# Performance work log

Measured on AMD Instinct MI355X. Metric: run time of the kernel, lower is better.

Reference implementation:

```python
import jax, jax.numpy as jnp
import numpy as np

OUT_F = 4096   # compressed rows; logical m = 2*OUT_F
IN_F = 2048    # compressed cols; logical k = 2*IN_F
BATCH = 4096   # n = input.shape[0]

# valid sorted 2-of-4 column patterns for 2:4 structured sparsity
_PAIR_LUT = jnp.array([[0, 1], [0, 2], [0, 3], [1, 2], [1, 3], [2, 3]], dtype=jnp.int32)


def setup_inputs() -> dict:
    key = jax.random.key(0)
    k1, k2, k3, k4 = jax.random.split(key, 4)
    weight = jax.random.normal(k1, (OUT_F, IN_F), dtype=jnp.float32)
    # vector (row) sparsity: keep 1 of every 2 logical row-vectors -> collision-free logical row ids
    row_bit = jax.random.randint(k2, (OUT_F,), 0, 2)
    indices = (2 * jnp.arange(OUT_F, dtype=jnp.int32) + row_bit.astype(jnp.int32))
    # 2:4 column sparsity: per group of 4 logical cols, keep 2 distinct sorted positions
    pat = jax.random.randint(k3, (OUT_F, IN_F // 2), 0, 6)
    metadata = _PAIR_LUT[pat].reshape(OUT_F, IN_F)  # [OUT_F, IN_F], values in 0..3
    inp = jax.random.normal(k4, (BATCH, 2 * IN_F), dtype=jnp.float32)
    return {"weight": weight, "indices": indices, "metadata": metadata, "input": inp}


def reference(weight, indices, metadata, input):
    # Decompress the dual structured-sparse weight to its logical dense form,
    # then compute W_logical @ input^T (spmm_dense_trans semantics).
    out_f, in_f = weight.shape
    m, k = 2 * out_f, 2 * in_f
    # logical column of each compressed element: group base 4*(c//2) + 2-bit metadata
    col = 4 * (jnp.arange(in_f, dtype=jnp.int32) // 2)[None, :] + metadata  # [out_f, in_f]
    W = jnp.zeros((m, k), dtype=weight.dtype).at[indices[:, None], col].set(weight)
    return W @ input.T  # [m, n] = [2*out_f, batch]
```

## Files before the change

### kernel.cpp

```cpp
#include <hip/hip_runtime.h>

#define OUT_F 4096
#define IN_F  2048
#define KLOG  4096
#define NB    4096
typedef unsigned long long ull;
typedef ull ullx2 __attribute__((ext_vector_type(2)));

typedef __bf16 bf16x8 __attribute__((ext_vector_type(8)));
typedef short  s16x8  __attribute__((ext_vector_type(8)));
typedef float  f32x4  __attribute__((ext_vector_type(4)));

__device__ __forceinline__ unsigned short f2bf(float f) {
    unsigned int u = __float_as_uint(f);
    u += 0x7fffu + ((u >> 16) & 1u);
    return (unsigned short)(u >> 16);
}

__device__ __forceinline__ void gload_lds16(const void* g, void* l) {
    __builtin_amdgcn_global_load_lds(
        (const __attribute__((address_space(1))) unsigned int*)g,
        (__attribute__((address_space(3))) unsigned int*)l, 16, 0, 0);
}

__device__ __forceinline__ bf16x8 ldsf(const char* p) {
    return __builtin_bit_cast(bf16x8, *(const s16x8*)p);
}

#define MFMA16(a, b, c) __builtin_amdgcn_mfma_f32_16x16x32_bf16((a), (b), (c), 0, 0, 0)

__global__ __launch_bounds__(256) void prep_kernel(
    const float* __restrict__ weight, const int* __restrict__ metadata,
    const float* __restrict__ input,
    unsigned short* __restrict__ wsA, unsigned short* __restrict__ wsB)
{
    const int b = blockIdx.x;
    if (b < 4096) {
        const int g = b * 256 + threadIdx.x;
        const int r = g >> 8;
        const int c = (g & 255) * 8;
        const size_t off = (size_t)r * IN_F + c;
        const float4 w0 = *(const float4*)(weight + off);
        const float4 w1 = *(const float4*)(weight + off + 4);
        const int4   m0 = *(const int4*)(metadata + off);
        const int4   m1 = *(const int4*)(metadata + off + 4);
        ullx2 v01, v23;
        v01.x = ((ull)f2bf(w0.x) << (m0.x * 16)) | ((ull)f2bf(w0.y) << (m0.y * 16));
        v01.y = ((ull)f2bf(w0.z) << (m0.z * 16)) | ((ull)f2bf(w0.w) << (m0.w * 16));
        v23.x = ((ull)f2bf(w1.x) << (m1.x * 16)) | ((ull)f2bf(w1.y) << (m1.y * 16));
        v23.y = ((ull)f2bf(w1.z) << (m1.z * 16)) | ((ull)f2bf(w1.w) << (m1.w * 16));
        ull* dst = (ull*)(wsA + (size_t)r * KLOG + 2 * c);
        *(ullx2*)(dst)     = v01;
        *(ullx2*)(dst + 2) = v23;
    } else {
        const int g = (b - 4096) * 256 + threadIdx.x;
        const size_t off = (size_t)g * 16;
        const float4 f0 = *(const float4*)(input + off);
        const float4 f1 = *(const float4*)(input + off + 4);
        const float4 f2 = *(const float4*)(input + off + 8);
        const float4 f3 = *(const float4*)(input + off + 12);
        ullx2 v01, v23;
        v01.x =  (ull)f2bf(f0.x) | ((ull)f2bf(f0.y) << 16) | ((ull)f2bf(f0.z) << 32) | ((ull)f2bf(f0.w) << 48);
        v01.y =  (ull)f2bf(f1.x) | ((ull)f2bf(f1.y) << 16) | ((ull)f2bf(f1.z) << 32) | ((ull)f2bf(f1.w) << 48);
        v23.x =  (ull)f2bf(f2.x) | ((ull)f2bf(f2.y) << 16) | ((ull)f2bf(f2.z) << 32) | ((ull)f2bf(f2.w) << 48);
        v23.y =  (ull)f2bf(f3.x) | ((ull)f2bf(f3.y) << 16) | ((ull)f2bf(f3.z) << 32) | ((ull)f2bf(f3.w) << 48);
        ull* dst = (ull*)(wsB + off);
        *(ullx2*)(dst)     = v01;
        *(ullx2*)(dst + 2) = v23;
    }
}

__global__ __launch_bounds__(512, 2) void gemm_kernel256(
    const unsigned short* __restrict__ wsA, const unsigned short* __restrict__ wsB,
    const int* __restrict__ indices, float* __restrict__ out)
{
    __shared__ __align__(16) char lds[4 * 32768];

    const int tid  = threadIdx.x;
    const int lane = tid & 63;
    const int wave = tid >> 6;
    const int wm   = wave >> 2;
    const int wn   = wave & 3;
    const int l15  = lane & 15;
    const int quad = lane >> 4;

    const int swz = ((blockIdx.x & 7) << 5) | (blockIdx.x >> 3);
    const int r0 = (swz >> 4) << 8;
    const int b0 = (swz & 15) << 8;

    const int srow   = tid >> 2;
    const int schunk = (tid & 3) ^ ((tid >> 3) & 3);
    const unsigned short* gA = wsA + (size_t)(r0 + srow) * KLOG + schunk * 8;
    const unsigned short* gB = wsB + (size_t)(b0 + srow) * KLOG + schunk * 8;
    char* const ldsW = lds + wave * 1024;

    const unsigned xq    = (unsigned)((quad ^ ((l15 >> 1) & 3)) * 16);
    const unsigned aBase = (unsigned)((wm * 128 + l15) * 64);
    const unsigned bBase = (unsigned)((wn * 64  + l15) * 64);

    f32x4 acc[8][4];
#pragma unroll
    for (int i = 0; i < 8; ++i)
#pragma unroll
        for (int j = 0; j < 4; ++j) acc[i][j] = (f32x4){0.f, 0.f, 0.f, 0.f};

#define STAGE_A(t_) do { \
        char* _d = ldsW + (((t_) & 3) * 32768); \
        const unsigned short* _s = gA + (t_) * 32; \
        gload_lds16(_s, _d); \
        gload_lds16(_s + (size_t)128 * KLOG, _d + 8192); } while (0)
#define STAGE_B(t_) do { \
        char* _d = ldsW + (((t_) & 3) * 32768) + 16384; \
        const unsigned short* _s = gB + (t_) * 32; \
        gload_lds16(_s, _d); \
        gload_lds16(_s + (size_t)128 * KLOG, _d + 8192); } while (0)

#define BAR()     __builtin_amdgcn_s_barrier()
#define SCHED0()  __builtin_amdgcn_sched_barrier(0)
#define LGKM0()   asm volatile("s_waitcnt lgkmcnt(0)" ::: "memory")

    STAGE_A(0); STAGE_B(0);
    STAGE_A(1); STAGE_B(1);
    STAGE_A(2); STAGE_B(2);
    asm volatile("s_waitcnt vmcnt(8)" ::: "memory");
    BAR();
    SCHED0();

    for (int t = 0; t < 128; ++t) {
        const unsigned bufO = (unsigned)(t & 3) * 32768u;
        const char* pA = lds + bufO + aBase;
        const char* pB = lds + bufO + 16384u + bBase;

        bf16x8 b0f = ldsf(pB + xq);
        bf16x8 b1f = ldsf(pB + 1024 + xq);
        bf16x8 b2f = ldsf(pB + 2048 + xq);
        bf16x8 b3f = ldsf(pB + 3072 + xq);
        bf16x8 a0 = ldsf(pA + xq);
        bf16x8 a1 = ldsf(pA + 1024 + xq);
        bf16x8 a2 = ldsf(pA + 2048 + xq);
        bf16x8 a3 = ldsf(pA + 3072 + xq);
        if (t < 125) STAGE_A(t + 3);
        BAR();
        LGKM0();
        SCHED0();
        __builtin_amdgcn_s_setprio(1);
        acc[0][0] = MFMA16(a0, b0f, acc[0][0]);
        acc[0][1] = MFMA16(a0, b1f, acc[0][1]);
        acc[0][2] = MFMA16(a0, b2f, acc[0][2]);
        acc[0][3] = MFMA16(a0, b3f, acc[0][3]);
        acc[1][0] = MFMA16(a1, b0f, acc[1][0]);
        acc[1][1] = MFMA16(a1, b1f, acc[1][1]);
        acc[1][2] = MFMA16(a1, b2f, acc[1][2]);
        acc[1][3] = MFMA16(a1, b3f, acc[1][3]);
        acc[2][0] = MFMA16(a2, b0f, acc[2][0]);
        acc[2][1] = MFMA16(a2, b1f, acc[2][1]);
        acc[2][2] = MFMA16(a2, b2f, acc[2][2]);
        acc[2][3] = MFMA16(a2, b3f, acc[2][3]);
        acc[3][0] = MFMA16(a3, b0f, acc[3][0]);
        acc[3][1] = MFMA16(a3, b1f, acc[3][1]);
        acc[3][2] = MFMA16(a3, b2f, acc[3][2]);
        acc[3][3] = MFMA16(a3, b3f, acc[3][3]);
        __builtin_amdgcn_s_setprio(0);
        BAR();
        SCHED0();

        bf16x8 a4 = ldsf(pA + 4096 + xq);
        bf16x8 a5 = ldsf(pA + 5120 + xq);
        bf16x8 a6 = ldsf(pA + 6144 + xq);
        bf16x8 a7 = ldsf(pA + 7168 + xq);
        if (t < 125) STAGE_B(t + 3);
        BAR();
        LGKM0();
        SCHED0();
        __builtin_amdgcn_s_setprio(1);
        acc[4][0] = MFMA16(a4, b0f, acc[4][0]);
        acc[4][1] = MFMA16(a4, b1f, acc[4][1]);
        acc[4][2] = MFMA16(a4, b2f, acc[4][2]);
        acc[4][3] = MFMA16(a4, b3f, acc[4][3]);
        acc[5][0] = MFMA16(a5, b0f, acc[5][0]);
        acc[5][1] = MFMA16(a5, b1f, acc[5][1]);
        acc[5][2] = MFMA16(a5, b2f, acc[5][2]);
        acc[5][3] = MFMA16(a5, b3f, acc[5][3]);
        acc[6][0] = MFMA16(a6, b0f, acc[6][0]);
        acc[6][1] = MFMA16(a6, b1f, acc[6][1]);
        acc[6][2] = MFMA16(a6, b2f, acc[6][2]);
        acc[6][3] = MFMA16(a6, b3f, acc[6][3]);
        acc[7][0] = MFMA16(a7, b0f, acc[7][0]);
        acc[7][1] = MFMA16(a7, b1f, acc[7][1]);
        acc[7][2] = MFMA16(a7, b2f, acc[7][2]);
        acc[7][3] = MFMA16(a7, b3f, acc[7][3]);
        __builtin_amdgcn_s_setprio(0);

        if (t < 125) {
            asm volatile("s_waitcnt vmcnt(8)" ::: "memory");
        } else if (t == 125) {
            asm volatile("s_waitcnt vmcnt(4)" ::: "memory");
        } else if (t == 126) {
            asm volatile("s_waitcnt vmcnt(0)" ::: "memory");
        }
        BAR();
        SCHED0();
    }
#undef STAGE_A
#undef STAGE_B
#undef BAR
#undef SCHED0
#undef LGKM0

#pragma unroll
    for (int rg = 0; rg < 8; ++rg) {
#pragma unroll
        for (int e = 0; e < 4; ++e) {
            const int rloc = wm * 128 + rg * 16 + quad * 4 + e;
            const int L = indices[r0 + rloc];
            const size_t base  = (size_t)L * NB;
            const size_t baseZ = (size_t)(L ^ 1) * NB;
#pragma unroll
            for (int cf = 0; cf < 4; ++cf) {
                const int col = b0 + wn * 64 + cf * 16 + l15;
                out[base  + col] = acc[rg][cf][e];
                out[baseZ + col] = 0.0f;
            }
        }
    }
}

__global__ __launch_bounds__(256) void spmm_dt_fallback(
    const float* __restrict__ weight, const int* __restrict__ indices,
    const int* __restrict__ metadata, const float* __restrict__ input,
    float* __restrict__ out)
{
    __shared__ __align__(16) unsigned short As[128][32];
    __shared__ __align__(16) unsigned short Bs[128][32];
    const int tid = threadIdx.x, lane = tid & 63, wave = tid >> 6;
    const int wm = wave >> 1, wn = wave & 1, l15 = lane & 15, quad = lane >> 4;
    const int r0 = blockIdx.y * 128, b0 = blockIdx.x * 128;
    f32x4 acc[4][4];
#pragma unroll
    for (int i = 0; i < 4; ++i)
#pragma unroll
        for (int j = 0; j < 4; ++j) acc[i][j] = (f32x4){0.f, 0.f, 0.f, 0.f};
    const int srow = tid >> 3, sgrp = tid & 7;
    for (int kk = 0; kk < KLOG / 32; ++kk) {
        const int c0 = kk * 16, k0 = kk * 32;
#pragma unroll
        for (int s = 0; s < 4; ++s) {
            const int row = srow + s * 32;
            const size_t off = (size_t)(r0 + row) * IN_F + c0 + 2 * sgrp;
            const float2 w = *(const float2*)(weight + off);
            const int2  md = *(const int2*)(metadata + off);
            *(ull*)(&As[row][4 * sgrp]) =
                ((ull)f2bf(w.x) << (md.x * 16)) | ((ull)f2bf(w.y) << (md.y * 16));
        }
#pragma unroll
        for (int s = 0; s < 4; ++s) {
            const int row = srow + s * 32;
            const float4 f = *(const float4*)(&input[(size_t)(b0 + row) * KLOG + k0 + sgrp * 4]);
            *(ull*)(&Bs[row][sgrp * 4]) =
                 (ull)f2bf(f.x) | ((ull)f2bf(f.y) << 16) |
                ((ull)f2bf(f.z) << 32) | ((ull)f2bf(f.w) << 48);
        }
        __syncthreads();
        bf16x8 a[4], b[4];
#pragma unroll
        for (int i = 0; i < 4; ++i)
            a[i] = __builtin_bit_cast(bf16x8, *(const s16x8*)(&As[wm * 64 + i * 16 + l15][quad * 8]));
#pragma unroll
        for (int j = 0; j < 4; ++j)
            b[j] = __builtin_bit_cast(bf16x8, *(const s16x8*)(&Bs[wn * 64 + j * 16 + l15][quad * 8]));
#pragma unroll
        for (int i = 0; i < 4; ++i)
#pragma unroll
            for (int j = 0; j < 4; ++j)
                acc[i][j] = __builtin_amdgcn_mfma_f32_16x16x32_bf16(a[i], b[j], acc[i][j], 0, 0, 0);
        __syncthreads();
    }
#pragma unroll
    for (int i = 0; i < 4; ++i)
#pragma unroll
        for (int t = 0; t < 4; ++t) {
            const int r = r0 + wm * 64 + i * 16 + quad * 4 + t;
            const int L = indices[r];
            const size_t base = (size_t)L * NB, baseZ = (size_t)(L ^ 1) * NB;
#pragma unroll
            for (int j = 0; j < 4; ++j) {
                const int col = b0 + wn * 64 + j * 16 + l15;
                out[base + col] = acc[i][j][t];
                out[baseZ + col] = 0.0f;
            }
        }
}

extern "C" void kernel_launch(void* const* d_in, const int* in_sizes, int n_in,
                              void* d_out, int out_size, void* d_ws, size_t ws_size,
                              hipStream_t stream) {
    const float* weight   = (const float*)d_in[0];
    const int*   indices  = (const int*)d_in[1];
    const int*   metadata = (const int*)d_in[2];
    const float* input    = (const float*)d_in[3];
    float*       out      = (float*)d_out;

    const size_t needA = (size_t)OUT_F * KLOG * 2;
    const size_t needB = (size_t)NB * KLOG * 2;
    if (ws_size >= needA + needB) {
        unsigned short* wsA = (unsigned short*)d_ws;
        unsigned short* wsB = wsA + (size_t)OUT_F * KLOG;
        prep_kernel<<<dim3(8192), dim3(256), 0, stream>>>(weight, metadata, input, wsA, wsB);
        gemm_kernel256<<<dim3(256), dim3(512), 0, stream>>>(wsA, wsB, indices, out);
    } else {
        spmm_dt_fallback<<<dim3(NB / 128, OUT_F / 128), dim3(256), 0, stream>>>(
            weight, indices, metadata, input, out);
    }
}
```

Baseline: 354.3 us.

## Pre-swizzle weight into MFMA fragment layout and load A directly to registers

The prep kernel now writes the decompressed bf16 weight in a fragment-ordered layout, so each lane's MFMA A operand is a contiguous 16-byte chunk. The GEMM then loads A straight from global memory into double-buffered registers instead of staging it through LDS, leaving only B in a halved LDS ring. The main loop becomes one barrier-synchronised phase per K tile instead of two. The intent is to cut LDS traffic, barriers and LDS footprint, at the cost of more registers and global-load latency that has to be hidden by the one-tile register prefetch.

```diff
diff --git a/kernel.cpp b/kernel.cpp
--- a/kernel.cpp
+++ b/kernel.cpp
@@ -27,6 +27,10 @@
     return __builtin_bit_cast(bf16x8, *(const s16x8*)p);
 }
 
+__device__ __forceinline__ bf16x8 gldf(const unsigned short* p) {
+    return __builtin_bit_cast(bf16x8, *(const s16x8*)p);
+}
+
 #define MFMA16(a, b, c) __builtin_amdgcn_mfma_f32_16x16x32_bf16((a), (b), (c), 0, 0, 0)
 
 __global__ __launch_bounds__(256) void prep_kernel(
@@ -35,25 +39,22 @@
     unsigned short* __restrict__ wsA, unsigned short* __restrict__ wsB)
 {
     const int b = blockIdx.x;
-    if (b < 4096) {
-        const int g = b * 256 + threadIdx.x;
-        const int r = g >> 8;
-        const int c = (g & 255) * 8;
-        const size_t off = (size_t)r * IN_F + c;
-        const float4 w0 = *(const float4*)(weight + off);
-        const float4 w1 = *(const float4*)(weight + off + 4);
-        const int4   m0 = *(const int4*)(metadata + off);
-        const int4   m1 = *(const int4*)(metadata + off + 4);
-        ullx2 v01, v23;
-        v01.x = ((ull)f2bf(w0.x) << (m0.x * 16)) | ((ull)f2bf(w0.y) << (m0.y * 16));
-        v01.y = ((ull)f2bf(w0.z) << (m0.z * 16)) | ((ull)f2bf(w0.w) << (m0.w * 16));
-        v23.x = ((ull)f2bf(w1.x) << (m1.x * 16)) | ((ull)f2bf(w1.y) << (m1.y * 16));
-        v23.y = ((ull)f2bf(w1.z) << (m1.z * 16)) | ((ull)f2bf(w1.w) << (m1.w * 16));
-        ull* dst = (ull*)(wsA + (size_t)r * KLOG + 2 * c);
-        *(ullx2*)(dst)     = v01;
-        *(ullx2*)(dst + 2) = v23;
+    if (b < 8192) {
+        const int R    = b >> 5;
+        const int lane = threadIdx.x & 63;
+        const int Kq   = ((b & 31) << 2) + (threadIdx.x >> 6);
+        const int row  = (R << 4) + (lane & 15);
+        const int kl0  = (Kq << 5) + (lane >> 4) * 8;
+        const int cc   = kl0 >> 1;
+        const size_t off = (size_t)row * IN_F + cc;
+        const float4 w = *(const float4*)(weight + off);
+        const int4  md = *(const int4*)(metadata + off);
+        ullx2 v;
+        v.x = ((ull)f2bf(w.x) << (md.x * 16)) | ((ull)f2bf(w.y) << (md.y * 16));
+        v.y = ((ull)f2bf(w.z) << (md.z * 16)) | ((ull)f2bf(w.w) << (md.w * 16));
+        *(ullx2*)(wsA + ((size_t)(R * 128 + Kq) * 64 + lane) * 8) = v;
     } else {
-        const int g = (b - 4096) * 256 + threadIdx.x;
+        const int g = (b - 8192) * 256 + threadIdx.x;
         const size_t off = (size_t)g * 16;
         const float4 f0 = *(const float4*)(input + off);
         const float4 f1 = *(const float4*)(input + off + 4);
@@ -71,10 +72,11 @@
 }
 
 __global__ __launch_bounds__(512, 2) void gemm_kernel256(
-    const unsigned short* __restrict__ wsA, const unsigned short* __restrict__ wsB,
+    const unsigned short* __restrict__ wsA,
+    const unsigned short* __restrict__ wsB,
     const int* __restrict__ indices, float* __restrict__ out)
 {
-    __shared__ __align__(16) char lds[4 * 32768];
+    __shared__ __align__(16) char lds[4 * 16384];
 
     const int tid  = threadIdx.x;
     const int lane = tid & 63;
@@ -90,13 +92,13 @@
 
     const int srow   = tid >> 2;
     const int schunk = (tid & 3) ^ ((tid >> 3) & 3);
-    const unsigned short* gA = wsA + (size_t)(r0 + srow) * KLOG + schunk * 8;
     const unsigned short* gB = wsB + (size_t)(b0 + srow) * KLOG + schunk * 8;
-    char* const ldsW = lds + wave * 1024;
 
     const unsigned xq    = (unsigned)((quad ^ ((l15 >> 1) & 3)) * 16);
-    const unsigned aBase = (unsigned)((wm * 128 + l15) * 64);
-    const unsigned bBase = (unsigned)((wn * 64  + l15) * 64);
+    const unsigned bBase = (unsigned)((wn * 64 + l15) * 64);
+
+    const unsigned short* aBase = wsA
+        + (size_t)((r0 >> 4) + wm * 8) * 128 * 512 + (unsigned)lane * 8;
 
     f32x4 acc[8][4];
 #pragma unroll
@@ -104,108 +106,92 @@
 #pragma unroll
         for (int j = 0; j < 4; ++j) acc[i][j] = (f32x4){0.f, 0.f, 0.f, 0.f};
 
-#define STAGE_A(t_) do { \
-        char* _d = ldsW + (((t_) & 3) * 32768); \
-        const unsigned short* _s = gA + (t_) * 32; \
-        gload_lds16(_s, _d); \
-        gload_lds16(_s + (size_t)128 * KLOG, _d + 8192); } while (0)
+    bf16x8 aP[8], aQ[8];
+
 #define STAGE_B(t_) do { \
-        char* _d = ldsW + (((t_) & 3) * 32768) + 16384; \
+        char* _d = lds + (((t_) & 3) * 16384) + wave * 1024; \
         const unsigned short* _s = gB + (t_) * 32; \
         gload_lds16(_s, _d); \
         gload_lds16(_s + (size_t)128 * KLOG, _d + 8192); } while (0)
 
+#define LOADA(D, t_) do { \
+        const unsigned short* _p = aBase + (size_t)(t_) * 512; \
+        D[0] = gldf(_p); \
+        D[1] = gldf(_p + 1 * 65536); \
+        D[2] = gldf(_p + 2 * 65536); \
+        D[3] = gldf(_p + 3 * 65536); \
+        D[4] = gldf(_p + 4 * 65536); \
+        D[5] = gldf(_p + 5 * 65536); \
+        D[6] = gldf(_p + 6 * 65536); \
+        D[7] = gldf(_p + 7 * 65536); } while (0)
+
 #define BAR()     __builtin_amdgcn_s_barrier()
 #define SCHED0()  __builtin_amdgcn_sched_barrier(0)
-#define LGKM0()   asm volatile("s_waitcnt lgkmcnt(0)" ::: "memory")
-
-    STAGE_A(0); STAGE_B(0);
-    STAGE_A(1); STAGE_B(1);
-    STAGE_A(2); STAGE_B(2);
-    asm volatile("s_waitcnt vmcnt(8)" ::: "memory");
+
+#define TILE(t_, CUR, NXT) do { \
+        if ((t_) < 127) LOADA(NXT, (t_) + 1); \
+        if ((t_) < 125) STAGE_B((t_) + 3); \
+        const char* pB = lds + ((unsigned)((t_) & 3)) * 16384u + bBase; \
+        bf16x8 bf0 = ldsf(pB + xq); \
+        bf16x8 bf1 = ldsf(pB + 1024 + xq); \
+        bf16x8 bf2 = ldsf(pB + 2048 + xq); \
+        bf16x8 bf3 = ldsf(pB + 3072 + xq); \
+        SCHED0(); \
+        __builtin_amdgcn_s_setprio(1); \
+        acc[0][0] = MFMA16(CUR[0], bf0, acc[0][0]); \
+        acc[0][1] = MFMA16(CUR[0], bf1, acc[0][1]); \
+        acc[0][2] = MFMA16(CUR[0], bf2, acc[0][2]); \
+        acc[0][3] = MFMA16(CUR[0], bf3, acc[0][3]); \
+        acc[1][0] = MFMA16(CUR[1], bf0, acc[1][0]); \
+        acc[1][1] = MFMA16(CUR[1], bf1, acc[1][1]); \
+        acc[1][2] = MFMA16(CUR[1], bf2, acc[1][2]); \
+        acc[1][3] = MFMA16(CUR[1], bf3, acc[1][3]); \
+        acc[2][0] = MFMA16(CUR[2], bf0, acc[2][0]); \
+        acc[2][1] = MFMA16(CUR[2], bf1, acc[2][1]); \
+        acc[2][2] = MFMA16(CUR[2], bf2, acc[2][2]); \
+        acc[2][3] = MFMA16(CUR[2], bf3, acc[2][3]); \
+        acc[3][0] = MFMA16(CUR[3], bf0, acc[3][0]); \
+        acc[3][1] = MFMA16(CUR[3], bf1, acc[3][1]); \
+        acc[3][2] = MFMA16(CUR[3], bf2, acc[3][2]); \
+        acc[3][3] = MFMA16(CUR[3], bf3, acc[3][3]); \
+        acc[4][0] = MFMA16(CUR[4], bf0, acc[4][0]); \
+        acc[4][1] = MFMA16(CUR[4], bf1, acc[4][1]); \
+        acc[4][2] = MFMA16(CUR[4], bf2, acc[4][2]); \
+        acc[4][3] = MFMA16(CUR[4], bf3, acc[4][3]); \
+        acc[5][0] = MFMA16(CUR[5], bf0, acc[5][0]); \
+        acc[5][1] = MFMA16(CUR[5], bf1, acc[5][1]); \
+        acc[5][2] = MFMA16(CUR[5], bf2, acc[5][2]); \
+        acc[5][3] = MFMA16(CUR[5], bf3, acc[5][3]); \
+        acc[6][0] = MFMA16(CUR[6], bf0, acc[6][0]); \
+        acc[6][1] = MFMA16(CUR[6], bf1, acc[6][1]); \
+        acc[6][2] = MFMA16(CUR[6], bf2, acc[6][2]); \
+        acc[6][3] = MFMA16(CUR[6], bf3, acc[6][3]); \
+        acc[7][0] = MFMA16(CUR[7], bf0, acc[7][0]); \
+        acc[7][1] = MFMA16(CUR[7], bf1, acc[7][1]); \
+        acc[7][2] = MFMA16(CUR[7], bf2, acc[7][2]); \
+        acc[7][3] = MFMA16(CUR[7], bf3, acc[7][3]); \
+        __builtin_amdgcn_s_setprio(0); \
+        if ((t_) < 125) { asm volatile("s_waitcnt vmcnt(2)" ::: "memory"); } \
+        else            { asm volatile("s_waitcnt vmcnt(0)" ::: "memory"); } \
+        BAR(); \
+        SCHED0(); } while (0)
+
+    LOADA(aP, 0);
+    STAGE_B(0); STAGE_B(1); STAGE_B(2);
+    asm volatile("s_waitcnt vmcnt(4)" ::: "memory");
     BAR();
     SCHED0();
 
-    for (int t = 0; t < 128; ++t) {
-        const unsigned bufO = (unsigned)(t & 3) * 32768u;
-        const char* pA = lds + bufO + aBase;
-        const char* pB = lds + bufO + 16384u + bBase;
-
-        bf16x8 b0f = ldsf(pB + xq);
-        bf16x8 b1f = ldsf(pB + 1024 + xq);
-        bf16x8 b2f = ldsf(pB + 2048 + xq);
-        bf16x8 b3f = ldsf(pB + 3072 + xq);
-        bf16x8 a0 = ldsf(pA + xq);
-        bf16x8 a1 = ldsf(pA + 1024 + xq);
-        bf16x8 a2 = ldsf(pA + 2048 + xq);
-        bf16x8 a3 = ldsf(pA + 3072 + xq);
-        if (t < 125) STAGE_A(t + 3);
-        BAR();
-        LGKM0();
-        SCHED0();
-        __builtin_amdgcn_s_setprio(1);
-        acc[0][0] = MFMA16(a0, b0f, acc[0][0]);
-        acc[0][1] = MFMA16(a0, b1f, acc[0][1]);
-        acc[0][2] = MFMA16(a0, b2f, acc[0][2]);
-        acc[0][3] = MFMA16(a0, b3f, acc[0][3]);
-        acc[1][0] = MFMA16(a1, b0f, acc[1][0]);
-        acc[1][1] = MFMA16(a1, b1f, acc[1][1]);
-        acc[1][2] = MFMA16(a1, b2f, acc[1][2]);
-        acc[1][3] = MFMA16(a1, b3f, acc[1][3]);
-        acc[2][0] = MFMA16(a2, b0f, acc[2][0]);
-        acc[2][1] = MFMA16(a2, b1f, acc[2][1]);
-        acc[2][2] = MFMA16(a2, b2f, acc[2][2]);
-        acc[2][3] = MFMA16(a2, b3f, acc[2][3]);
-        acc[3][0] = MFMA16(a3, b0f, acc[3][0]);
-        acc[3][1] = MFMA16(a3, b1f, acc[3][1]);
-        acc[3][2] = MFMA16(a3, b2f, acc[3][2]);
-        acc[3][3] = MFMA16(a3, b3f, acc[3][3]);
-        __builtin_amdgcn_s_setprio(0);
-        BAR();
-        SCHED0();
-
-        bf16x8 a4 = ldsf(pA + 4096 + xq);
-        bf16x8 a5 = ldsf(pA + 5120 + xq);
-        bf16x8 a6 = ldsf(pA + 6144 + xq);
-        bf16x8 a7 = ldsf(pA + 7168 + xq);
-        if (t < 125) STAGE_B(t + 3);
-        BAR();
-        LGKM0();
-        SCHED0();
-        __builtin_amdgcn_s_setprio(1);
-        acc[4][0] = MFMA16(a4, b0f, acc[4][0]);
-        acc[4][1] = MFMA16(a4, b1f, acc[4][1]);
-        acc[4][2] = MFMA16(a4, b2f, acc[4][2]);
-        acc[4][3] = MFMA16(a4, b3f, acc[4][3]);
-        acc[5][0] = MFMA16(a5, b0f, acc[5][0]);
-        acc[5][1] = MFMA16(a5, b1f, acc[5][1]);
-        acc[5][2] = MFMA16(a5, b2f, acc[5][2]);
-        acc[5][3] = MFMA16(a5, b3f, acc[5][3]);
-        acc[6][0] = MFMA16(a6, b0f, acc[6][0]);
-        acc[6][1] = MFMA16(a6, b1f, acc[6][1]);
-        acc[6][2] = MFMA16(a6, b2f, acc[6][2]);
-        acc[6][3] = MFMA16(a6, b3f, acc[6][3]);
-        acc[7][0] = MFMA16(a7, b0f, acc[7][0]);
-        acc[7][1] = MFMA16(a7, b1f, acc[7][1]);
-        acc[7][2] = MFMA16(a7, b2f, acc[7][2]);
-        acc[7][3] = MFMA16(a7, b3f, acc[7][3]);
-        __builtin_amdgcn_s_setprio(0);
-
-        if (t < 125) {
-            asm volatile("s_waitcnt vmcnt(8)" ::: "memory");
-        } else if (t == 125) {
-            asm volatile("s_waitcnt vmcnt(4)" ::: "memory");
-        } else if (t == 126) {
-            asm volatile("s_waitcnt vmcnt(0)" ::: "memory");
-        }
-        BAR();
-        SCHED0();
-    }
-#undef STAGE_A
+    for (int i = 0; i < 64; ++i) {
+        const int ta = 2 * i, tb = 2 * i + 1;
+        TILE(ta, aP, aQ);
+        TILE(tb, aQ, aP);
+    }
 #undef STAGE_B
+#undef LOADA
 #undef BAR
 #undef SCHED0
-#undef LGKM0
+#undef TILE
 
 #pragma unroll
     for (int rg = 0; rg < 8; ++rg) {
@@ -305,7 +291,7 @@
     if (ws_size >= needA + needB) {
         unsigned short* wsA = (unsigned short*)d_ws;
         unsigned short* wsB = wsA + (size_t)OUT_F * KLOG;
-        prep_kernel<<<dim3(8192), dim3(256), 0, stream>>>(weight, metadata, input, wsA, wsB);
+        prep_kernel<<<dim3(12288), dim3(256), 0, stream>>>(weight, metadata, input, wsA, wsB);
         gemm_kernel256<<<dim3(256), dim3(512), 0, stream>>>(wsA, wsB, indices, out);
     } else {
         spmm_dt_fallback<<<dim3(NB / 128, OUT_F / 128), dim3(256), 0, stream>>>(
```

Measured after the change: 376.8 us. +6.4%, slower.
